# Performance work log

Measured on AMD Instinct MI355X. Metric: run time of the kernel, lower is better.

Reference implementation:

```python
import jax, jax.numpy as jnp
import numpy as np

VOCAB, EMB, HID, OUT = 32000, 512, 1024, 2
B, T = 64, 512


def setup_inputs() -> dict:
    key = jax.random.key(0)
    ks = jax.random.split(key, 12)
    def xavier(k, shape):
        fan_in, fan_out = shape
        lim = np.sqrt(6.0 / (fan_in + fan_out)).astype(np.float32)
        return jax.random.uniform(k, shape, jnp.float32, -lim, lim)
    x = jax.random.randint(ks[0], (B, T), 0, VOCAB, dtype=jnp.int32)
    emb = jax.random.uniform(ks[1], (VOCAB, EMB), jnp.float32, -0.1, 0.1)
    inp = {
        "x": x,
        "emb": emb,
        "Wxi": xavier(ks[2], (EMB, HID)), "Whi": xavier(ks[3], (HID, HID)), "bi": jnp.zeros((HID,), jnp.float32),
        "Wxf": xavier(ks[4], (EMB, HID)), "Whf": xavier(ks[5], (HID, HID)), "bf": jnp.zeros((HID,), jnp.float32),
        "Wxc": xavier(ks[6], (EMB, HID)), "Whc": xavier(ks[7], (HID, HID)), "bc": jnp.zeros((HID,), jnp.float32),
        "Wxo": xavier(ks[8], (EMB, HID)), "Who": xavier(ks[9], (HID, HID)), "bo": jnp.zeros((HID,), jnp.float32),
        "Why": xavier(ks[10], (HID, OUT)), "by": jnp.zeros((OUT,), jnp.float32),
    }
    return inp


def reference(x, emb, Wxi, Whi, bi, Wxf, Whf, bf, Wxc, Whc, bc, Wxo, Who, bo, Why, by):
    # Embedding lookup: [B, T, E]
    xe = emb[x]
    # Precompute input projections for all 4 gates in one batched contraction each.
    # Stack Wx matrices -> [E, 4H]; gates_x: [T, B, 4H] (time-major for scan)
    Wx = jnp.concatenate([Wxi, Wxf, Wxc, Wxo], axis=1)          # [E, 4H]
    Wh = jnp.concatenate([Whi, Whf, Whc, Who], axis=1)          # [H, 4H]
    b = jnp.concatenate([bi, bf, bc, bo], axis=0)               # [4H]
    gates_x = jnp.einsum('bte,eg->tbg', xe, Wx)                  # [T, B, 4H]
    H = Whi.shape[0]

    def step(carry, gx):
        h, c = carry
        g = gx + h @ Wh + b                                      # [B, 4H]
        i = jax.nn.sigmoid(g[:, 0 * H:1 * H])
        f = jax.nn.sigmoid(g[:, 1 * H:2 * H])
        gg = jnp.tanh(g[:, 2 * H:3 * H])
        o = jax.nn.sigmoid(g[:, 3 * H:4 * H])
        c = f * c + i * gg
        h = o * jnp.tanh(c)
        return (h, c), None

    h0 = jnp.zeros((x.shape[0], H), xe.dtype)
    c0 = jnp.zeros((x.shape[0], H), xe.dtype)
    (h, c), _ = jax.lax.scan(step, (h0, c0), gates_x)
    # dropout is identity in eval mode
    return h @ Why + by
```

## Files before the change

### kernel.cpp

```cpp
#include <hip/hip_runtime.h>

#define TT 512
#define BB 64
#define EMB 512
#define HID 1024
#define K4 1536
#define NBLK 256
#define THREADS 256

typedef __bf16 bf16x8 __attribute__((ext_vector_type(8)));
typedef float f32x4 __attribute__((ext_vector_type(4)));

__device__ __forceinline__ unsigned short f2bf(float f) {
    union { float f; unsigned u; } v; v.f = f;
    unsigned u = v.u;
    unsigned r = u + 0x7FFFu + ((u >> 16) & 1u);
    return (unsigned short)(r >> 16);
}

__global__ void zero_kernel(unsigned* p, int n) {
    int i = blockIdx.x * 256 + threadIdx.x;
    if (i < n) p[i] = 0u;
}

__global__ void xe_kernel(const int* __restrict__ x, const float* __restrict__ emb,
                          unsigned short* __restrict__ xe_all) {
    int rowid = blockIdx.x;
    int t = rowid >> 6, b = rowid & 63;
    int idx = x[b * TT + t];
    float4 v = ((const float4*)(emb + (long)idx * EMB))[threadIdx.x];
    ushort4 o;
    o.x = f2bf(v.x); o.y = f2bf(v.y); o.z = f2bf(v.z); o.w = f2bf(v.w);
    ((ushort4*)(xe_all + (long)rowid * EMB))[threadIdx.x] = o;
}

__global__ void wpack_kernel(const float* __restrict__ Wxi, const float* __restrict__ Whi,
                             const float* __restrict__ Wxf, const float* __restrict__ Whf,
                             const float* __restrict__ Wxc, const float* __restrict__ Whc,
                             const float* __restrict__ Wxo, const float* __restrict__ Who,
                             unsigned short* __restrict__ Wpack) {
    const float* Wx[4] = {Wxi, Wxf, Wxc, Wxo};
    const float* Wh[4] = {Whi, Whf, Whc, Who};
    int n0 = (blockIdx.x & 15) << 8;
    int k0 = (blockIdx.x >> 4) << 3;
    int g = n0 >> 10, col0 = n0 & 1023;
    const float* base = (k0 < 512) ? (Wx[g] + (long)k0 * HID + col0)
                                   : (Wh[g] + (long)(k0 - 512) * HID + col0);
    int tid = threadIdx.x;
    union { unsigned short s[8]; uint4 v; } out;
#pragma unroll
    for (int i = 0; i < 8; ++i) out.s[i] = f2bf(base[(long)i * HID + tid]);
    *(uint4*)(Wpack + (long)(n0 + tid) * K4 + k0) = out.v;
}

#define MFMA(a, b, c) __builtin_amdgcn_mfma_f32_16x16x32_bf16((a), (b), (c), 0, 0, 0)

__launch_bounds__(THREADS, 1)
__global__ void lstm_kernel(const unsigned short* __restrict__ xe_all,
                            const unsigned short* __restrict__ Wpack,
                            unsigned short* __restrict__ hbuf,
                            float* __restrict__ hfinal,
                            unsigned* __restrict__ arrive,
                            const float* __restrict__ bi_p, const float* __restrict__ bf_p,
                            const float* __restrict__ bc_p, const float* __restrict__ bo_p) {
    __shared__ unsigned short Wlds[32 * 1536];
    __shared__ __align__(16) float partials[4][32][44];

    const int tid = threadIdx.x;
    const int wave = tid >> 6, lane = tid & 63;
    const int quad = lane >> 4, r16 = lane & 15;
    const int ks4 = wave;
    const int bid = blockIdx.x;
    const int half = bid & 1;
    const int j0 = (bid >> 1) * 8;

#pragma unroll
    for (int i = 0; i < 24; ++i) {
        int gidx = tid + i * THREADS;
        int c = gidx / 192, q = gidx % 192;
        int n = ((c >> 3) << 10) + j0 + (c & 7);
        *(uint4*)(&Wlds[(c * 192 + (q ^ (c & 7))) * 8]) =
            *(const uint4*)(Wpack + (long)n * K4 + q * 8);
    }
    const int b_loc = tid >> 3, jj = tid & 7;
    const int b_ = half * 32 + b_loc;
    float rb0 = bi_p[j0 + jj], rb1 = bf_p[j0 + jj], rb2 = bc_p[j0 + jj], rb3 = bo_p[j0 + jj];
    float c_state = 0.f;
    __syncthreads();

    const f32x4 zf = {0.f, 0.f, 0.f, 0.f};
    const int row0 = half * 32 + r16;
    const int s0 = r16 & 7;

    for (int t = 0; t < TT; ++t) {
        const unsigned short* xe_t = xe_all + (long)t * (BB * EMB);
        const unsigned short* hb = hbuf + (t & 1) * (BB * HID);

        f32x4 acc00 = zf, acc01 = zf, acc10 = zf, acc11 = zf;

        {
            uint4 xa[4][2];
#pragma unroll
            for (int i = 0; i < 4; ++i) {
                int k = ks4 * 128 + i * 32 + quad * 8;
                xa[i][0] = *(const uint4*)(xe_t + (long)row0 * EMB + k);
                xa[i][1] = *(const uint4*)(xe_t + (long)(row0 + 16) * EMB + k);
            }
#pragma unroll
            for (int i = 0; i < 4; ++i) {
                int bk = (ks4 * 128 + i * 32 + quad * 8) >> 3;
                bf16x8 b0 = *(const bf16x8*)(&Wlds[(r16 * 192 + (bk ^ s0)) * 8]);
                bf16x8 b1 = *(const bf16x8*)(&Wlds[((16 + r16) * 192 + (bk ^ s0)) * 8]);
                bf16x8 a0 = __builtin_bit_cast(bf16x8, xa[i][0]);
                bf16x8 a1 = __builtin_bit_cast(bf16x8, xa[i][1]);
                acc00 = MFMA(a0, b0, acc00); acc01 = MFMA(a0, b1, acc01);
                acc10 = MFMA(a1, b0, acc10); acc11 = MFMA(a1, b1, acc11);
            }
        }

        if (t > 0) {
            const unsigned* fp = &arrive[((t - 1) * 16 + half * 8 + (lane & 7)) * 16];
            while (!__all(__hip_atomic_load(fp, __ATOMIC_RELAXED,
                                            __HIP_MEMORY_SCOPE_AGENT) >= 16u))
                __builtin_amdgcn_s_sleep(1);
            asm volatile("" ::: "memory");
        }

        {
            uint4 ha[8][2];
#pragma unroll
            for (int i = 0; i < 8; ++i) {
                const unsigned short* p0 = hb + (long)row0 * HID + ks4 * 256 + i * 32 + quad * 8;
                const unsigned short* p1 = p0 + 16 * HID;
                asm volatile("global_load_dwordx4 %0, %1, off sc1" : "=v"(ha[i][0]) : "v"(p0));
                asm volatile("global_load_dwordx4 %0, %1, off sc1" : "=v"(ha[i][1]) : "v"(p1));
            }
            asm volatile("s_waitcnt vmcnt(0)" ::: "memory");
#pragma unroll
            for (int i = 0; i < 8; ++i) {
                int bk = (512 + ks4 * 256 + i * 32 + quad * 8) >> 3;
                bf16x8 b0 = *(const bf16x8*)(&Wlds[(r16 * 192 + (bk ^ s0)) * 8]);
                bf16x8 b1 = *(const bf16x8*)(&Wlds[((16 + r16) * 192 + (bk ^ s0)) * 8]);
                bf16x8 a0 = __builtin_bit_cast(bf16x8, ha[i][0]);
                bf16x8 a1 = __builtin_bit_cast(bf16x8, ha[i][1]);
                acc00 = MFMA(a0, b0, acc00); acc01 = MFMA(a0, b1, acc01);
                acc10 = MFMA(a1, b0, acc10); acc11 = MFMA(a1, b1, acc11);
            }
        }

        {
            int pr0 = quad * 4;
            *(f32x4*)&partials[ks4][r16][pr0]           = acc00;
            *(f32x4*)&partials[ks4][16 + r16][pr0]      = acc01;
            *(f32x4*)&partials[ks4][r16][pr0 + 16]      = acc10;
            *(f32x4*)&partials[ks4][16 + r16][pr0 + 16] = acc11;
        }
        __syncthreads();

        float gi = 0.f, gf = 0.f, gc = 0.f, go = 0.f;
#pragma unroll
        for (int w = 0; w < 4; ++w) {
            gi += partials[w][jj][b_loc];
            gf += partials[w][8 + jj][b_loc];
            gc += partials[w][16 + jj][b_loc];
            go += partials[w][24 + jj][b_loc];
        }
        gi += rb0; gf += rb1; gc += rb2; go += rb3;
        float si = 1.f / (1.f + __expf(-gi));
        float sf = 1.f / (1.f + __expf(-gf));
        float so = 1.f / (1.f + __expf(-go));
        float e2 = __expf(2.f * gc); float tc = (e2 - 1.f) / (e2 + 1.f);
        float c = sf * c_state + si * tc;
        c_state = c;
        float e2c = __expf(2.f * c); float th = (e2c - 1.f) / (e2c + 1.f);
        float h = so * th;

        unsigned short hv = f2bf(h);
        const unsigned short* hop = hbuf + ((t + 1) & 1) * (BB * HID) + b_ * HID + j0 + jj;
        asm volatile("global_store_short %0, %1, off sc1" :: "v"(hop), "v"(hv) : "memory");
        if (t == TT - 1) hfinal[b_ * HID + j0 + jj] = h;
        asm volatile("s_waitcnt vmcnt(0)" ::: "memory");
        __syncthreads();
        if (tid == 0)
            __hip_atomic_fetch_add(&arrive[(t * 16 + half * 8 + ((bid >> 1) & 7)) * 16], 1u,
                                   __ATOMIC_RELAXED, __HIP_MEMORY_SCOPE_AGENT);
    }
}

__global__ void out_kernel(const float* __restrict__ hfinal, const float* __restrict__ Why,
                           const float* __restrict__ by, float* __restrict__ y) {
    int gw = blockIdx.x * 4 + (threadIdx.x >> 6);
    int lane = threadIdx.x & 63;
    int b = gw >> 1, o = gw & 1;
    float s = 0.f;
    for (int k = lane; k < HID; k += 64) s += hfinal[b * HID + k] * Why[k * 2 + o];
#pragma unroll
    for (int off = 32; off; off >>= 1) s += __shfl_down(s, off);
    if (lane == 0) y[b * 2 + o] = s + by[o];
}

extern "C" void kernel_launch(void* const* d_in, const int* in_sizes, int n_in,
                              void* d_out, int out_size, void* d_ws, size_t ws_size,
                              hipStream_t stream) {
    const int*   x   = (const int*)d_in[0];
    const float* emb = (const float*)d_in[1];
    const float* Wxi = (const float*)d_in[2];
    const float* Whi = (const float*)d_in[3];
    const float* bi  = (const float*)d_in[4];
    const float* Wxf = (const float*)d_in[5];
    const float* Whf = (const float*)d_in[6];
    const float* bfp = (const float*)d_in[7];
    const float* Wxc = (const float*)d_in[8];
    const float* Whc = (const float*)d_in[9];
    const float* bc  = (const float*)d_in[10];
    const float* Wxo = (const float*)d_in[11];
    const float* Who = (const float*)d_in[12];
    const float* bo  = (const float*)d_in[13];
    const float* Why = (const float*)d_in[14];
    const float* by  = (const float*)d_in[15];
    float* y = (float*)d_out;

    char* ws = (char*)d_ws;
    unsigned short* Wpack  = (unsigned short*)ws;
    unsigned short* xe_all = (unsigned short*)(ws + 12582912);
    unsigned short* hbuf   = (unsigned short*)(ws + 12582912 + 33554432);
    unsigned*       arrive = (unsigned*)(ws + 12582912 + 33554432 + 262144);
    float*          hfinal = (float*)(ws + 12582912 + 33554432 + 262144 + 524288);

    zero_kernel<<<768, 256, 0, stream>>>((unsigned*)hbuf, 196608);
    wpack_kernel<<<3072, 256, 0, stream>>>(Wxi, Whi, Wxf, Whf, Wxc, Whc, Wxo, Who, Wpack);
    xe_kernel<<<32768, 128, 0, stream>>>(x, emb, xe_all);

    const unsigned short* xe_p = xe_all;
    const unsigned short* Wp_p = Wpack;
    unsigned short* hb_p = hbuf;
    float* hf_p = hfinal;
    unsigned* ar_p = arrive;
    void* args[] = {&xe_p, &Wp_p, &hb_p, &hf_p, &ar_p,
                    (void*)&bi, (void*)&bfp, (void*)&bc, (void*)&bo};
    hipLaunchCooperativeKernel((void*)lstm_kernel, dim3(NBLK), dim3(THREADS), args, 0, stream);

    out_kernel<<<32, 256, 0, stream>>>(hfinal, Why, by, y);
}
```

Measured before the change: 2.626 ms.

## Split LSTM step across 8 waves and wait only on needed h-slice counters

Doubles the block to 512 threads so each wave computes 16 batch rows instead of 32, halving per-wave MFMA and global-load work on the serial recurrent path. The arrival counters are regrouped by contiguous hidden-column ranges, so each wave waits only for the two counters covering the 256 h columns it reads, rather than for all producers of its half. The gate nonlinearities stay on the first 256 threads. The cost is more block-level sync participants and extra B-operand LDS reads, since both M-waves read the same weights.

```diff
diff --git a/kernel.cpp b/kernel.cpp
--- a/kernel.cpp
+++ b/kernel.cpp
@@ -6,7 +6,7 @@
 #define HID 1024
 #define K4 1536
 #define NBLK 256
-#define THREADS 256
+#define THREADS 512
 
 typedef __bf16 bf16x8 __attribute__((ext_vector_type(8)));
 typedef float f32x4 __attribute__((ext_vector_type(4)));
@@ -55,7 +55,7 @@
 
 #define MFMA(a, b, c) __builtin_amdgcn_mfma_f32_16x16x32_bf16((a), (b), (c), 0, 0, 0)
 
-__launch_bounds__(THREADS, 1)
+__launch_bounds__(THREADS, 2)
 __global__ void lstm_kernel(const unsigned short* __restrict__ xe_all,
                             const unsigned short* __restrict__ Wpack,
                             unsigned short* __restrict__ hbuf,
@@ -69,57 +69,60 @@
     const int tid = threadIdx.x;
     const int wave = tid >> 6, lane = tid & 63;
     const int quad = lane >> 4, r16 = lane & 15;
-    const int ks4 = wave;
+    const int ks4 = wave >> 1;
+    const int mw = wave & 1;
     const int bid = blockIdx.x;
     const int half = bid & 1;
-    const int j0 = (bid >> 1) * 8;
-
-#pragma unroll
-    for (int i = 0; i < 24; ++i) {
+    const int pidx = bid >> 1;
+    const int j0 = pidx * 8;
+
+#pragma unroll
+    for (int i = 0; i < 12; ++i) {
         int gidx = tid + i * THREADS;
         int c = gidx / 192, q = gidx % 192;
         int n = ((c >> 3) << 10) + j0 + (c & 7);
         *(uint4*)(&Wlds[(c * 192 + (q ^ (c & 7))) * 8]) =
             *(const uint4*)(Wpack + (long)n * K4 + q * 8);
     }
-    const int b_loc = tid >> 3, jj = tid & 7;
+    const int b_loc = (tid & 255) >> 3, jj = tid & 7;
     const int b_ = half * 32 + b_loc;
-    float rb0 = bi_p[j0 + jj], rb1 = bf_p[j0 + jj], rb2 = bc_p[j0 + jj], rb3 = bo_p[j0 + jj];
+    float rb0 = 0.f, rb1 = 0.f, rb2 = 0.f, rb3 = 0.f;
+    if (tid < 256) {
+        rb0 = bi_p[j0 + jj]; rb1 = bf_p[j0 + jj];
+        rb2 = bc_p[j0 + jj]; rb3 = bo_p[j0 + jj];
+    }
     float c_state = 0.f;
     __syncthreads();
 
     const f32x4 zf = {0.f, 0.f, 0.f, 0.f};
-    const int row0 = half * 32 + r16;
+    const int row0 = half * 32 + mw * 16 + r16;
     const int s0 = r16 & 7;
 
     for (int t = 0; t < TT; ++t) {
         const unsigned short* xe_t = xe_all + (long)t * (BB * EMB);
         const unsigned short* hb = hbuf + (t & 1) * (BB * HID);
 
-        f32x4 acc00 = zf, acc01 = zf, acc10 = zf, acc11 = zf;
+        f32x4 acc0 = zf, acc1 = zf;
 
         {
-            uint4 xa[4][2];
+            uint4 xa[4];
 #pragma unroll
             for (int i = 0; i < 4; ++i) {
                 int k = ks4 * 128 + i * 32 + quad * 8;
-                xa[i][0] = *(const uint4*)(xe_t + (long)row0 * EMB + k);
-                xa[i][1] = *(const uint4*)(xe_t + (long)(row0 + 16) * EMB + k);
+                xa[i] = *(const uint4*)(xe_t + (long)row0 * EMB + k);
             }
 #pragma unroll
             for (int i = 0; i < 4; ++i) {
                 int bk = (ks4 * 128 + i * 32 + quad * 8) >> 3;
                 bf16x8 b0 = *(const bf16x8*)(&Wlds[(r16 * 192 + (bk ^ s0)) * 8]);
                 bf16x8 b1 = *(const bf16x8*)(&Wlds[((16 + r16) * 192 + (bk ^ s0)) * 8]);
-                bf16x8 a0 = __builtin_bit_cast(bf16x8, xa[i][0]);
-                bf16x8 a1 = __builtin_bit_cast(bf16x8, xa[i][1]);
-                acc00 = MFMA(a0, b0, acc00); acc01 = MFMA(a0, b1, acc01);
-                acc10 = MFMA(a1, b0, acc10); acc11 = MFMA(a1, b1, acc11);
+                bf16x8 a0 = __builtin_bit_cast(bf16x8, xa[i]);
+                acc0 = MFMA(a0, b0, acc0); acc1 = MFMA(a0, b1, acc1);
             }
         }
 
         if (t > 0) {
-            const unsigned* fp = &arrive[((t - 1) * 16 + half * 8 + (lane & 7)) * 16];
+            const unsigned* fp = &arrive[((t - 1) * 16 + half * 8 + ks4 * 2 + (lane & 1)) * 16];
             while (!__all(__hip_atomic_load(fp, __ATOMIC_RELAXED,
                                             __HIP_MEMORY_SCOPE_AGENT) >= 16u))
                 __builtin_amdgcn_s_sleep(1);
@@ -127,13 +130,11 @@
         }
 
         {
-            uint4 ha[8][2];
+            uint4 ha[8];
 #pragma unroll
             for (int i = 0; i < 8; ++i) {
                 const unsigned short* p0 = hb + (long)row0 * HID + ks4 * 256 + i * 32 + quad * 8;
-                const unsigned short* p1 = p0 + 16 * HID;
-                asm volatile("global_load_dwordx4 %0, %1, off sc1" : "=v"(ha[i][0]) : "v"(p0));
-                asm volatile("global_load_dwordx4 %0, %1, off sc1" : "=v"(ha[i][1]) : "v"(p1));
+                asm volatile("global_load_dwordx4 %0, %1, off sc1" : "=v"(ha[i]) : "v"(p0));
             }
             asm volatile("s_waitcnt vmcnt(0)" ::: "memory");
 #pragma unroll
@@ -141,48 +142,45 @@
                 int bk = (512 + ks4 * 256 + i * 32 + quad * 8) >> 3;
                 bf16x8 b0 = *(const bf16x8*)(&Wlds[(r16 * 192 + (bk ^ s0)) * 8]);
                 bf16x8 b1 = *(const bf16x8*)(&Wlds[((16 + r16) * 192 + (bk ^ s0)) * 8]);
-                bf16x8 a0 = __builtin_bit_cast(bf16x8, ha[i][0]);
-                bf16x8 a1 = __builtin_bit_cast(bf16x8, ha[i][1]);
-                acc00 = MFMA(a0, b0, acc00); acc01 = MFMA(a0, b1, acc01);
-                acc10 = MFMA(a1, b0, acc10); acc11 = MFMA(a1, b1, acc11);
+                bf16x8 a0 = __builtin_bit_cast(bf16x8, ha[i]);
+                acc0 = MFMA(a0, b0, acc0); acc1 = MFMA(a0, b1, acc1);
             }
         }
 
         {
-            int pr0 = quad * 4;
-            *(f32x4*)&partials[ks4][r16][pr0]           = acc00;
-            *(f32x4*)&partials[ks4][16 + r16][pr0]      = acc01;
-            *(f32x4*)&partials[ks4][r16][pr0 + 16]      = acc10;
-            *(f32x4*)&partials[ks4][16 + r16][pr0 + 16] = acc11;
+            int pm = mw * 16 + quad * 4;
+            *(f32x4*)&partials[ks4][r16][pm]      = acc0;
+            *(f32x4*)&partials[ks4][16 + r16][pm] = acc1;
         }
         __syncthreads();
 
-        float gi = 0.f, gf = 0.f, gc = 0.f, go = 0.f;
-#pragma unroll
-        for (int w = 0; w < 4; ++w) {
-            gi += partials[w][jj][b_loc];
-            gf += partials[w][8 + jj][b_loc];
-            gc += partials[w][16 + jj][b_loc];
-            go += partials[w][24 + jj][b_loc];
-        }
-        gi += rb0; gf += rb1; gc += rb2; go += rb3;
-        float si = 1.f / (1.f + __expf(-gi));
-        float sf = 1.f / (1.f + __expf(-gf));
-        float so = 1.f / (1.f + __expf(-go));
-        float e2 = __expf(2.f * gc); float tc = (e2 - 1.f) / (e2 + 1.f);
-        float c = sf * c_state + si * tc;
-        c_state = c;
-        float e2c = __expf(2.f * c); float th = (e2c - 1.f) / (e2c + 1.f);
-        float h = so * th;
-
-        unsigned short hv = f2bf(h);
-        const unsigned short* hop = hbuf + ((t + 1) & 1) * (BB * HID) + b_ * HID + j0 + jj;
-        asm volatile("global_store_short %0, %1, off sc1" :: "v"(hop), "v"(hv) : "memory");
-        if (t == TT - 1) hfinal[b_ * HID + j0 + jj] = h;
+        if (tid < 256) {
+            float gi = 0.f, gf = 0.f, gc = 0.f, go = 0.f;
+#pragma unroll
+            for (int w = 0; w < 4; ++w) {
+                gi += partials[w][jj][b_loc];
+                gf += partials[w][8 + jj][b_loc];
+                gc += partials[w][16 + jj][b_loc];
+                go += partials[w][24 + jj][b_loc];
+            }
+            gi += rb0; gf += rb1; gc += rb2; go += rb3;
+            float si = 1.f / (1.f + __expf(-gi));
+            float sf = 1.f / (1.f + __expf(-gf));
+            float so = 1.f / (1.f + __expf(-go));
+            float e2 = __expf(2.f * gc); float tc = (e2 - 1.f) / (e2 + 1.f);
+            float c = sf * c_state + si * tc;
+            c_state = c;
+            float e2c = __expf(2.f * c); float th = (e2c - 1.f) / (e2c + 1.f);
+            float h = so * th;
+            unsigned short hv = f2bf(h);
+            const unsigned short* hop = hbuf + ((t + 1) & 1) * (BB * HID) + b_ * HID + j0 + jj;
+            asm volatile("global_store_short %0, %1, off sc1" :: "v"(hop), "v"(hv) : "memory");
+            if (t == TT - 1) hfinal[b_ * HID + j0 + jj] = h;
+        }
         asm volatile("s_waitcnt vmcnt(0)" ::: "memory");
         __syncthreads();
         if (tid == 0)
-            __hip_atomic_fetch_add(&arrive[(t * 16 + half * 8 + ((bid >> 1) & 7)) * 16], 1u,
+            __hip_atomic_fetch_add(&arrive[(t * 16 + half * 8 + (pidx >> 4)) * 16], 1u,
                                    __ATOMIC_RELAXED, __HIP_MEMORY_SCOPE_AGENT);
     }
 }
```

Measured after the change: 2.412 ms. 8.1% less time.
